# Optimization experiments

Hardware: AMD Instinct MI355X
Metric: run time of the kernel (lower is better)

Reference implementation:

```python
import jax, jax.numpy as jnp
import numpy as np

B, IN_DIM, HID, PROJ, OUT = 32768, 4097, 2048, 512, 3
FEAT = IN_DIM - 1
EPS = 1e-12  # F.normalize eps


def setup_inputs() -> dict:
    key = jax.random.key(0)
    ks = jax.random.split(key, 16)
    x_feat = jax.random.normal(ks[0], (B, FEAT), dtype=jnp.float32)
    flag = jax.random.randint(ks[1], (B, 1), 0, 2).astype(jnp.float32)
    x = jnp.concatenate([x_feat, flag], axis=1)  # [B, IN_DIM], last col is 0/1 flag

    def lin(k, fan_in, fan_out):
        bound = 1.0 / np.sqrt(fan_in)
        kw, kb = jax.random.split(k)
        W = jax.random.uniform(kw, (fan_in, fan_out), jnp.float32, -bound, bound)
        b = jax.random.uniform(kb, (fan_out,), jnp.float32, -bound, bound)
        return W, b

    W1n, b1n = lin(ks[2], FEAT, HID)
    W2n, b2n = lin(ks[3], HID, PROJ)
    Wcn, bcn = lin(ks[4], PROJ, OUT)
    W1o, b1o = lin(ks[5], FEAT, HID)
    W2o, b2o = lin(ks[6], HID, PROJ)
    Wco, bco = lin(ks[7], PROJ, OUT)
    return {"x": x, "W1n": W1n, "b1n": b1n, "W2n": W2n, "b2n": b2n,
            "Wcn": Wcn, "bcn": bcn, "W1o": W1o, "b1o": b1o, "W2o": W2o,
            "b2o": b2o, "Wco": Wco, "bco": bco}


def _path(feat, W1, b1, W2, b2):
    # Linear -> ReLU -> Dropout(eval: identity) -> Linear
    h = jax.nn.relu(feat @ W1 + b1)
    return h @ W2 + b2  # [B, PROJ]


def reference(x, W1n, b1n, W2n, b2n, Wcn, bcn, W1o, b1o, W2o, b2o, Wco, bco):
    flag = x[:, -1:] > 0.5          # [B,1] bool; 1 -> natural path
    feat = x[:, :-1]                # [B, FEAT]
    # Dense 2-expert compute + select (same math as gather/scatter routing).
    z_nat = _path(feat, W1n, b1n, W2n, b2n)
    z_oth = _path(feat, W1o, b1o, W2o, b2o)
    z = jnp.where(flag, z_nat, z_oth)                      # [B, PROJ]
    logits_nat = jax.nn.relu(z_nat) @ Wcn + bcn
    logits_oth = jax.nn.relu(z_oth) @ Wco + bco
    logits = jnp.where(flag, logits_nat, logits_oth)       # [B, OUT]
    norm = jnp.linalg.norm(z, axis=1, keepdims=True)
    z_normalized = z / jnp.maximum(norm, EPS)
    return (z_normalized, logits)
```

## Files before the change

### kernel.cpp

```cpp
#include <hip/hip_runtime.h>
#include <hip/hip_bf16.h>

typedef __bf16 bf16_t;
typedef __attribute__((ext_vector_type(8))) __bf16 bf16x8;
typedef __attribute__((ext_vector_type(4))) __bf16 bf16x4;
typedef __attribute__((ext_vector_type(4))) float f32x4;

#define NROWS 32768
#define FEAT  4096
#define INDIM 4097
#define HID   2048
#define PROJ  512
#define NPAD  33024
#define MTILES 258
#define SENT  0xFFFFFFFFu

__device__ __forceinline__ void load_lds16(const bf16_t* g, char* s) {
  __builtin_amdgcn_global_load_lds(
      (__attribute__((address_space(1))) void*)(void*)g,
      (__attribute__((address_space(3))) void*)s, 16, 0, 0);
}

__global__ __launch_bounds__(256) void init_kernel(unsigned* __restrict__ perm,
                                                   int* __restrict__ cnt) {
  int i = blockIdx.x * 256 + threadIdx.x;
  if (i < NPAD) perm[i] = SENT;
  if (i < 4) cnt[i] = 0;
}

__global__ __launch_bounds__(256) void count_kernel(const float* __restrict__ x,
                                                    int* __restrict__ cnt) {
  int i = blockIdx.x * 256 + threadIdx.x;
  if (i >= NROWS) return;
  float f = x[(long)i * INDIM + FEAT];
  if (f > 0.5f) atomicAdd(&cnt[0], 1);
}

__global__ __launch_bounds__(256) void scatter_kernel(const float* __restrict__ x,
                                                      unsigned* __restrict__ perm,
                                                      int* __restrict__ cnt) {
  int i = blockIdx.x * 256 + threadIdx.x;
  if (i >= NROWS) return;
  float f = x[(long)i * INDIM + FEAT];
  int g = (f > 0.5f) ? 0 : 1;
  int pos = atomicAdd(&cnt[1 + g], 1);
  int off_oth = ((cnt[0] + 127) >> 7) << 7;
  int q = (g == 0) ? pos : off_oth + pos;
  perm[q] = (unsigned)i;
}

__global__ __launch_bounds__(256) void convert_x_kernel(const float* __restrict__ x,
                                                        bf16_t* __restrict__ xbf) {
  const int lane = threadIdx.x & 63;
  const long wid = ((long)blockIdx.x * 256 + threadIdx.x) >> 6;
  const long chunk = wid * 512;
  const long row = chunk >> 12;
  const long col = chunk & 4095;
  const float* src = x + row * INDIM + col + lane;
  bf16_t* dst = xbf + chunk + lane;
#pragma unroll
  for (int j = 0; j < 8; ++j)
    dst[j * 64] = (bf16_t)src[j * 64];
}

__global__ __launch_bounds__(256) void transpose_convert_kernel(
    const float* __restrict__ W, bf16_t* __restrict__ Wt, int K, int N) {
  __shared__ float tile[32][33];
  const int n0 = blockIdx.x << 5;
  const int k0 = blockIdx.y << 5;
  const int t = threadIdx.x;
  const int r = t >> 3;
  const int c4 = (t & 7) << 2;
  f32x4 v = *(const f32x4*)(W + (long)(k0 + r) * N + n0 + c4);
#pragma unroll
  for (int i = 0; i < 4; ++i) tile[r][c4 + i] = v[i];
  __syncthreads();
  bf16x4 o;
#pragma unroll
  for (int i = 0; i < 4; ++i) o[i] = (bf16_t)tile[c4 + i][r];
  *(bf16x4*)(Wt + (long)(n0 + r) * K + k0 + c4) = o;
}

template <bool GATHER, bool RELU_BF16>
__global__ __launch_bounds__(256) void gemm_kernel(
    const bf16_t* __restrict__ A,
    const bf16_t* __restrict__ BtNat, const bf16_t* __restrict__ BtOth,
    const float* __restrict__ biasNat, const float* __restrict__ biasOth,
    void* __restrict__ Cout,
    const unsigned* __restrict__ perm, const int* __restrict__ cnt,
    const int K, const int N) {
  __shared__ char smem[16384];
  const int tid = threadIdx.x;
  const int tile_m = blockIdx.y;
  const int qbase = tile_m << 7;
  if (perm[qbase] == SENT) return;
  const int n0 = blockIdx.x << 7;
  const int n_nat = cnt[0];
  const int m_tiles_nat = (n_nat + 127) >> 7;
  const bool nat = (tile_m < m_tiles_nat);
  const bf16_t* __restrict__ Bt = nat ? BtNat : BtOth;
  const float* __restrict__ bias = nat ? biasNat : biasOth;

  const int r0 = tid >> 2;
  const int kc = tid & 3;
  long arow0, arow1;
  if (GATHER) {
    unsigned p0 = perm[qbase + r0];
    unsigned p1 = perm[qbase + r0 + 64];
    arow0 = (p0 == SENT) ? 0 : (long)p0;
    arow1 = (p1 == SENT) ? 0 : (long)p1;
  } else {
    arow0 = qbase + r0;
    arow1 = qbase + r0 + 64;
  }
  const bf16_t* srcA0 = A + arow0 * K + (kc << 3);
  const bf16_t* srcA1 = A + arow1 * K + (kc << 3);
  const bf16_t* srcB0 = Bt + (long)(n0 + r0) * K + (kc << 3);
  const bf16_t* srcB1 = Bt + (long)(n0 + r0 + 64) * K + (kc << 3);

  const int wave = tid >> 6;
  const int lane = tid & 63;
  const int quad = lane >> 4;
  const int l16 = lane & 15;
  const int wm = (wave >> 1) << 6;
  const int wn = (wave & 1) << 6;

  char* const Alds = smem;
  char* const Blds = smem + 8192;
  char* const dstA0 = Alds + (wave << 10);
  char* const dstA1 = Alds + 4096 + (wave << 10);
  char* const dstB0 = Blds + (wave << 10);
  char* const dstB1 = Blds + 4096 + (wave << 10);

  f32x4 acc[4][4] = {};

  const int kiters = K >> 5;
  for (int kt = 0; kt < kiters; ++kt) {
    __syncthreads();
    load_lds16(srcA0, dstA0);
    load_lds16(srcA1, dstA1);
    load_lds16(srcB0, dstB0);
    load_lds16(srcB1, dstB1);
    srcA0 += 32; srcA1 += 32; srcB0 += 32; srcB1 += 32;
    __syncthreads();
    bf16x8 af[4], bfr[4];
#pragma unroll
    for (int i = 0; i < 4; ++i)
      af[i] = *(const bf16x8*)(Alds + (((wm + (i << 4) + l16) << 5) + (quad << 3)) * 2);
#pragma unroll
    for (int i = 0; i < 4; ++i)
      bfr[i] = *(const bf16x8*)(Blds + (((wn + (i << 4) + l16) << 5) + (quad << 3)) * 2);
#pragma unroll
    for (int mi = 0; mi < 4; ++mi)
#pragma unroll
      for (int ni = 0; ni < 4; ++ni)
        acc[mi][ni] = __builtin_amdgcn_mfma_f32_16x16x32_bf16(af[mi], bfr[ni], acc[mi][ni], 0, 0, 0);
  }

  float bv[4];
#pragma unroll
  for (int ni = 0; ni < 4; ++ni) bv[ni] = bias[n0 + wn + (ni << 4) + l16];

#pragma unroll
  for (int mi = 0; mi < 4; ++mi) {
#pragma unroll
    for (int ni = 0; ni < 4; ++ni) {
#pragma unroll
      for (int r = 0; r < 4; ++r) {
        const int m = wm + (mi << 4) + (quad << 2) + r;
        const int col = n0 + wn + (ni << 4) + l16;
        float v = acc[mi][ni][r] + bv[ni];
        if (RELU_BF16) {
          v = fmaxf(v, 0.0f);
          ((bf16_t*)Cout)[(long)(qbase + m) * N + col] = (bf16_t)v;
        } else {
          ((float*)Cout)[(long)(qbase + m) * N + col] = v;
        }
      }
    }
  }
}

__global__ __launch_bounds__(256) void epilogue_kernel(
    const float* __restrict__ z,
    const float* __restrict__ Wc0, const float* __restrict__ bc0,
    const float* __restrict__ Wc1, const float* __restrict__ bc1,
    const unsigned* __restrict__ perm, const int* __restrict__ cnt,
    float* __restrict__ out_z, float* __restrict__ out_logits) {
  __shared__ float WcL[2][PROJ * 3];
  for (int i = threadIdx.x; i < PROJ * 3; i += 256) {
    WcL[0][i] = Wc0[i];
    WcL[1][i] = Wc1[i];
  }
  __syncthreads();
  const int wave = threadIdx.x >> 6;
  const int lane = threadIdx.x & 63;
  const int q = blockIdx.x * 4 + wave;
  const unsigned orig = perm[q];
  if (orig == SENT) return;
  const int n_nat = cnt[0];
  const int off_oth = ((n_nat + 127) >> 7) << 7;
  const int g = (q < off_oth) ? 0 : 1;

  float zv[8];
  float ss = 0.f, l0 = 0.f, l1 = 0.f, l2 = 0.f;
#pragma unroll
  for (int i = 0; i < 8; ++i) {
    const int k = i * 64 + lane;
    float v = z[(long)q * PROJ + k];
    zv[i] = v;
    ss += v * v;
    float r = fmaxf(v, 0.f);
    const float* w = &WcL[g][k * 3];
    l0 += r * w[0];
    l1 += r * w[1];
    l2 += r * w[2];
  }
#pragma unroll
  for (int off = 32; off > 0; off >>= 1) {
    ss += __shfl_xor(ss, off);
    l0 += __shfl_xor(l0, off);
    l1 += __shfl_xor(l1, off);
    l2 += __shfl_xor(l2, off);
  }
  const float inv = 1.f / fmaxf(sqrtf(ss), 1e-12f);
#pragma unroll
  for (int i = 0; i < 8; ++i)
    out_z[(long)orig * PROJ + i * 64 + lane] = zv[i] * inv;
  if (lane == 0) {
    const float* bc = g ? bc1 : bc0;
    out_logits[(long)orig * 3 + 0] = l0 + bc[0];
    out_logits[(long)orig * 3 + 1] = l1 + bc[1];
    out_logits[(long)orig * 3 + 2] = l2 + bc[2];
  }
}

extern "C" void kernel_launch(void* const* d_in, const int* in_sizes, int n_in,
                              void* d_out, int out_size, void* d_ws, size_t ws_size,
                              hipStream_t stream) {
  const float* x   = (const float*)d_in[0];
  const float* W1n = (const float*)d_in[1];
  const float* b1n = (const float*)d_in[2];
  const float* W2n = (const float*)d_in[3];
  const float* b2n = (const float*)d_in[4];
  const float* Wcn = (const float*)d_in[5];
  const float* bcn = (const float*)d_in[6];
  const float* W1o = (const float*)d_in[7];
  const float* b1o = (const float*)d_in[8];
  const float* W2o = (const float*)d_in[9];
  const float* b2o = (const float*)d_in[10];
  const float* Wco = (const float*)d_in[11];
  const float* bco = (const float*)d_in[12];

  char* ws = (char*)d_ws;
  bf16_t* xbf  = (bf16_t*)ws;
  float*  z_ws = (float*)ws;
  size_t off = 268435456;
  bf16_t* W1tn = (bf16_t*)(ws + off); off += (size_t)FEAT * HID * 2;
  bf16_t* W1to = (bf16_t*)(ws + off); off += (size_t)FEAT * HID * 2;
  bf16_t* W2tn = (bf16_t*)(ws + off); off += (size_t)HID * PROJ * 2;
  bf16_t* W2to = (bf16_t*)(ws + off); off += (size_t)HID * PROJ * 2;
  bf16_t* h_ws = (bf16_t*)(ws + off); off += (size_t)NPAD * HID * 2;
  unsigned* perm = (unsigned*)(ws + off); off += (size_t)NPAD * 4;
  int* cnt = (int*)(ws + off);

  float* out_z = (float*)d_out;
  float* out_logits = out_z + (size_t)NROWS * PROJ;

  init_kernel<<<(NPAD + 255) / 256, 256, 0, stream>>>(perm, cnt);
  count_kernel<<<NROWS / 256, 256, 0, stream>>>(x, cnt);
  scatter_kernel<<<NROWS / 256, 256, 0, stream>>>(x, perm, cnt);

  convert_x_kernel<<<(int)(((long)NROWS * FEAT / 512) / 4), 256, 0, stream>>>(x, xbf);
  transpose_convert_kernel<<<dim3(HID / 32, FEAT / 32), 256, 0, stream>>>(W1n, W1tn, FEAT, HID);
  transpose_convert_kernel<<<dim3(HID / 32, FEAT / 32), 256, 0, stream>>>(W1o, W1to, FEAT, HID);
  transpose_convert_kernel<<<dim3(PROJ / 32, HID / 32), 256, 0, stream>>>(W2n, W2tn, HID, PROJ);
  transpose_convert_kernel<<<dim3(PROJ / 32, HID / 32), 256, 0, stream>>>(W2o, W2to, HID, PROJ);

  gemm_kernel<true, true><<<dim3(HID / 128, MTILES), 256, 0, stream>>>(
      xbf, W1tn, W1to, b1n, b1o, (void*)h_ws, perm, cnt, FEAT, HID);

  gemm_kernel<false, false><<<dim3(PROJ / 128, MTILES), 256, 0, stream>>>(
      h_ws, W2tn, W2to, b2n, b2o, (void*)z_ws, perm, cnt, HID, PROJ);

  epilogue_kernel<<<NPAD / 4, 256, 0, stream>>>(
      z_ws, Wcn, bcn, Wco, bco, perm, cnt, out_z, out_logits);
}
```

Measured before the change: 1.998 ms.

## Reorganize GEMM LDS layout to k-chunk-major and vectorize x conversion stores

The GEMM tile staging changes from a row-major [row][32 k] LDS layout to a k-chunk-major layout. Each wave now loads one 8-element k-chunk for 64 consecutive rows, and the MFMA fragment reads index by (quad, row). The intent is to remove LDS bank conflicts on the fragment reads and to need one perm lookup per thread instead of two. Separately, the x fp32-to-bf16 conversion now has each thread write one 16-byte bf16x8 vector, at the cost of uncoalesced strided fp32 loads per thread, since rows of length 4097 are not 16-byte aligned.

```diff
diff --git a/kernel.cpp b/kernel.cpp
--- a/kernel.cpp
+++ b/kernel.cpp
@@ -51,16 +51,15 @@
 
 __global__ __launch_bounds__(256) void convert_x_kernel(const float* __restrict__ x,
                                                         bf16_t* __restrict__ xbf) {
-  const int lane = threadIdx.x & 63;
-  const long wid = ((long)blockIdx.x * 256 + threadIdx.x) >> 6;
-  const long chunk = wid * 512;
-  const long row = chunk >> 12;
-  const long col = chunk & 4095;
-  const float* src = x + row * INDIM + col + lane;
-  bf16_t* dst = xbf + chunk + lane;
-#pragma unroll
-  for (int j = 0; j < 8; ++j)
-    dst[j * 64] = (bf16_t)src[j * 64];
+  const long t = (long)blockIdx.x * 256 + threadIdx.x;
+  const long o = t << 3;
+  const long row = o >> 12;
+  const long col = o & 4095;
+  const float* src = x + row * INDIM + col;
+  bf16x8 v;
+#pragma unroll
+  for (int j = 0; j < 8; ++j) v[j] = (bf16_t)src[j];
+  *(bf16x8*)(xbf + o) = v;
 }
 
 __global__ __launch_bounds__(256) void transpose_convert_kernel(
@@ -101,25 +100,23 @@
   const bf16_t* __restrict__ Bt = nat ? BtNat : BtOth;
   const float* __restrict__ bias = nat ? biasNat : biasOth;
 
-  const int r0 = tid >> 2;
-  const int kc = tid & 3;
-  long arow0, arow1;
-  if (GATHER) {
-    unsigned p0 = perm[qbase + r0];
-    unsigned p1 = perm[qbase + r0 + 64];
-    arow0 = (p0 == SENT) ? 0 : (long)p0;
-    arow1 = (p1 == SENT) ? 0 : (long)p1;
-  } else {
-    arow0 = qbase + r0;
-    arow1 = qbase + r0 + 64;
-  }
-  const bf16_t* srcA0 = A + arow0 * K + (kc << 3);
-  const bf16_t* srcA1 = A + arow1 * K + (kc << 3);
-  const bf16_t* srcB0 = Bt + (long)(n0 + r0) * K + (kc << 3);
-  const bf16_t* srcB1 = Bt + (long)(n0 + r0 + 64) * K + (kc << 3);
-
   const int wave = tid >> 6;
   const int lane = tid & 63;
+
+  const int srow = ((wave & 1) << 6) + lane;
+  const int kc0 = wave >> 1;
+  long arow;
+  if (GATHER) {
+    unsigned p = perm[qbase + srow];
+    arow = (p == SENT) ? 0 : (long)p;
+  } else {
+    arow = qbase + srow;
+  }
+  const bf16_t* srcA0 = A + arow * K + (kc0 << 3);
+  const bf16_t* srcA1 = srcA0 + 16;
+  const bf16_t* srcB0 = Bt + (long)(n0 + srow) * K + (kc0 << 3);
+  const bf16_t* srcB1 = srcB0 + 16;
+
   const int quad = lane >> 4;
   const int l16 = lane & 15;
   const int wm = (wave >> 1) << 6;
@@ -128,9 +125,9 @@
   char* const Alds = smem;
   char* const Blds = smem + 8192;
   char* const dstA0 = Alds + (wave << 10);
-  char* const dstA1 = Alds + 4096 + (wave << 10);
+  char* const dstA1 = Alds + ((wave + 4) << 10);
   char* const dstB0 = Blds + (wave << 10);
-  char* const dstB1 = Blds + 4096 + (wave << 10);
+  char* const dstB1 = Blds + ((wave + 4) << 10);
 
   f32x4 acc[4][4] = {};
 
@@ -146,10 +143,10 @@
     bf16x8 af[4], bfr[4];
 #pragma unroll
     for (int i = 0; i < 4; ++i)
-      af[i] = *(const bf16x8*)(Alds + (((wm + (i << 4) + l16) << 5) + (quad << 3)) * 2);
+      af[i] = *(const bf16x8*)(Alds + (((quad << 7) + wm + (i << 4) + l16) << 4));
 #pragma unroll
     for (int i = 0; i < 4; ++i)
-      bfr[i] = *(const bf16x8*)(Blds + (((wn + (i << 4) + l16) << 5) + (quad << 3)) * 2);
+      bfr[i] = *(const bf16x8*)(Blds + (((quad << 7) + wn + (i << 4) + l16) << 4));
 #pragma unroll
     for (int mi = 0; mi < 4; ++mi)
 #pragma unroll
@@ -271,7 +268,7 @@
   count_kernel<<<NROWS / 256, 256, 0, stream>>>(x, cnt);
   scatter_kernel<<<NROWS / 256, 256, 0, stream>>>(x, perm, cnt);
 
-  convert_x_kernel<<<(int)(((long)NROWS * FEAT / 512) / 4), 256, 0, stream>>>(x, xbf);
+  convert_x_kernel<<<(int)((long)NROWS * FEAT / 8 / 256), 256, 0, stream>>>(x, xbf);
   transpose_convert_kernel<<<dim3(HID / 32, FEAT / 32), 256, 0, stream>>>(W1n, W1tn, FEAT, HID);
   transpose_convert_kernel<<<dim3(HID / 32, FEAT / 32), 256, 0, stream>>>(W1o, W1to, FEAT, HID);
   transpose_convert_kernel<<<dim3(PROJ / 32, HID / 32), 256, 0, stream>>>(W2n, W2tn, HID, PROJ);
```

New measurement: 2.495 ms. +24.8%, slower.
